# Optimization experiments

Hardware: AMD Instinct MI355X
Metric: run time of the kernel (lower is better)

The kernel has to match this reference:

```python
import jax, jax.numpy as jnp
import numpy as np

B, N, DIM, H = 8, 2048, 64, 8  # per-head dim == DIM (module convention: inner_dim = dim * n_heads)


def setup_inputs() -> dict:
    key = jax.random.key(0)
    k1, k2, k3 = jax.random.split(key, 3)
    x = jax.random.normal(k1, (B, N, DIM), dtype=jnp.float32)
    W_qkv = jax.random.normal(k2, (DIM, 3 * H * DIM), dtype=jnp.float32) * (DIM ** -0.5)
    W_out = jax.random.normal(k3, (H * DIM, DIM), dtype=jnp.float32) * ((H * DIM) ** -0.5)
    b_out = jnp.zeros((DIM,), dtype=jnp.float32)
    return {"x": x, "W_qkv": W_qkv, "W_out": W_out, "b_out": b_out}


def reference(x, W_qkv, W_out, b_out):
    b, n, d = x.shape
    h = W_qkv.shape[1] // (3 * d)
    qkv = x @ W_qkv                                   # [b, n, 3*h*d]
    q, k, v = jnp.split(qkv, 3, axis=-1)              # each [b, n, h*d]
    def to_heads(t):
        return t.reshape(b, n, h, d).transpose(0, 2, 1, 3)  # [b, h, n, d]
    q, k, v = map(to_heads, (q, k, v))
    scale = d ** -0.5
    dot = jnp.einsum('bhid,bhjd->bhij', q, k) * scale  # [b, h, n, n]
    A = jax.nn.softmax(dot, axis=-1)
    z = jnp.einsum('bhij,bhjd->bhid', A, v)            # [b, h, n, d]
    z = z.transpose(0, 2, 1, 3).reshape(b, n, h * d)   # [b, n, h*d]
    return z @ W_out + b_out                           # [b, n, d]
```

## Files before the change

### kernel.cpp

```cpp
#include <hip/hip_runtime.h>
#include <math.h>

#define BB 8
#define NN 2048
#define DD 64
#define HH 8
#define BH (BB*HH)
#define HD (HH*DD)
#define NROWS (BB*NN)
#define QKV_COLS (3*HD)

typedef __bf16 bf16_8 __attribute__((ext_vector_type(8)));
typedef __bf16 bf16_4 __attribute__((ext_vector_type(4)));
typedef float  f32_16 __attribute__((ext_vector_type(16)));
typedef float  f32_4  __attribute__((ext_vector_type(4)));
typedef int    i32_2  __attribute__((ext_vector_type(2)));

#define QSCALE 0.180336880111f

__device__ __forceinline__ unsigned pack_bf16(float a, float b) {
  union { __bf16 h[2]; unsigned u; } t;
  t.h[0] = (__bf16)a; t.h[1] = (__bf16)b;
  return t.u;
}

__device__ __forceinline__ float fast_exp2(float x) {
#if __has_builtin(__builtin_amdgcn_exp2f)
  return __builtin_amdgcn_exp2f(x);
#else
  return __expf(x * 0.69314718056f);
#endif
}

__device__ __forceinline__ bf16_8 half_swap(unsigned a0, unsigned a1,
                                            unsigned a2, unsigned a3,
                                            int lhi, int xl) {
  union { unsigned u[4]; bf16_8 v; } F;
#if __has_builtin(__builtin_amdgcn_permlane32_swap)
  i32_2 r02 = __builtin_amdgcn_permlane32_swap((int)a0, (int)a2, false, false);
  i32_2 r13 = __builtin_amdgcn_permlane32_swap((int)a1, (int)a3, false, false);
  F.u[0] = (unsigned)r02.x; F.u[2] = (unsigned)r02.y;
  F.u[1] = (unsigned)r13.x; F.u[3] = (unsigned)r13.y;
#else
  unsigned w0 = (unsigned)__shfl((int)a0, xl, 64);
  unsigned w1 = (unsigned)__shfl((int)a1, xl, 64);
  unsigned w2 = (unsigned)__shfl((int)a2, xl, 64);
  unsigned w3 = (unsigned)__shfl((int)a3, xl, 64);
  F.u[0] = lhi ? w2 : a0;
  F.u[1] = lhi ? w3 : a1;
  F.u[2] = lhi ? a2 : w0;
  F.u[3] = lhi ? a3 : w1;
#endif
  return F.v;
}

__global__ __launch_bounds__(256) void qkv_kernel(
    const float* __restrict__ x, const float* __restrict__ Wqkv,
    const float* __restrict__ Wout,
    __bf16* __restrict__ Q, __bf16* __restrict__ K, __bf16* __restrict__ Vt,
    __bf16* __restrict__ Wob) {
  __shared__ __bf16 T[4][64][34];

  if (blockIdx.y == (NROWS / 128)) {
    int id = blockIdx.x * 256 + threadIdx.x;
    for (int e = id; e < 512 * 64; e += 24 * 256) {
      int kf = e >> 6, col = e & 63;
      int s = kf >> 4, lh = (kf >> 3) & 1, j = kf & 7;
      int t = col >> 5, lc = col & 31;
      Wob[((size_t)((t * 32 + s) * 64 + lh * 32 + lc)) * 8 + j] = (__bf16)Wout[e];
    }
    return;
  }

  const int lane = threadIdx.x & 63;
  const int wave = threadIdx.x >> 6;
  const int l31  = lane & 31, lhi = lane >> 5;
  const int cg   = blockIdx.x;
  const int row0 = blockIdx.y * 128 + wave * 32;

  const float* xr = x + (size_t)(row0 + l31) * 64 + lhi * 8;
  bf16_8 af[4];
#pragma unroll
  for (int s = 0; s < 4; s++) {
    f32_4 a0 = *(const f32_4*)(xr + s * 16);
    f32_4 a1 = *(const f32_4*)(xr + s * 16 + 4);
#pragma unroll
    for (int j = 0; j < 4; j++) { af[s][j] = (__bf16)a0[j]; af[s][4 + j] = (__bf16)a1[j]; }
  }

  const int col0  = cg * 64;
  const int which = col0 >> 9;
  const float wscl = (which == 0) ? QSCALE : 1.0f;

  f32_16 C0, C1;
#pragma unroll
  for (int i = 0; i < 16; i++) { C0[i] = 0.f; C1[i] = 0.f; }

#pragma unroll
  for (int s = 0; s < 4; s++) {
    bf16_8 b0, b1;
#pragma unroll
    for (int j = 0; j < 8; j++) {
      int k = s * 16 + lhi * 8 + j;
      b0[j] = (__bf16)(Wqkv[(size_t)k * QKV_COLS + col0 + l31]      * wscl);
      b1[j] = (__bf16)(Wqkv[(size_t)k * QKV_COLS + col0 + 32 + l31] * wscl);
    }
    C0 = __builtin_amdgcn_mfma_f32_32x32x16_bf16(af[s], b0, C0, 0, 0, 0);
    C1 = __builtin_amdgcn_mfma_f32_32x32x16_bf16(af[s], b1, C1, 0, 0, 0);
  }

  const int h   = (col0 >> 6) & 7;
  const int b   = row0 >> 11;
  const int n0l = row0 & 2047;

  if (which < 2) {
    __bf16* dst = (which == 0) ? Q : K;
#pragma unroll
    for (int r = 0; r < 16; r++) {
      int nl = (r & 3) + 8 * (r >> 2) + 4 * lhi;
      size_t base = (((size_t)(b * HH + h) * NN) + n0l + nl) * DD;
      dst[base + l31]      = (__bf16)C0[r];
      dst[base + 32 + l31] = (__bf16)C1[r];
    }
  } else {
    __bf16 (*Tw)[34] = T[wave];
#pragma unroll
    for (int r = 0; r < 16; r++) {
      int nl = (r & 3) + 8 * (r >> 2) + 4 * lhi;
      Tw[l31][nl]      = (__bf16)C0[r];
      Tw[32 + l31][nl] = (__bf16)C1[r];
    }
    __bf16* dst = Vt + (((size_t)(b * HH + h) * DD) + lane) * NN + n0l;
#pragma unroll
    for (int j = 0; j < 4; j++) {
      *(bf16_8*)(dst + j * 8) = *(const bf16_8*)(&Tw[lane][j * 8]);
    }
  }
}

#define TILE_ELEMS (128 * 72 + 64 * 136)
__global__ __launch_bounds__(512) void attn_kernel(
    const __bf16* __restrict__ Q, const __bf16* __restrict__ K,
    const __bf16* __restrict__ Vt, __bf16* __restrict__ z) {
  __shared__ __bf16 SMEM[2][TILE_ELEMS];

  const int tid  = threadIdx.x;
  const int wave = tid >> 6;
  const int lane = tid & 63;
  const int l31  = lane & 31;
  const int lhi  = lane >> 5;
  const int xl   = lane ^ 32;
  const int bh   = blockIdx.x >> 2;
  const int q0   = (blockIdx.x & 3) * 512 + wave * 64;

  const __bf16* Qbase = Q + ((size_t)bh * NN + q0 + l31) * DD + lhi * 8;
  bf16_8 qfa[4], qfb[4];
#pragma unroll
  for (int s = 0; s < 4; s++) {
    qfa[s] = *(const bf16_8*)(Qbase + s * 16);
    qfb[s] = *(const bf16_8*)(Qbase + (size_t)32 * DD + s * 16);
  }

  f32_16 O0a, O1a, O0b, O1b;
#pragma unroll
  for (int i = 0; i < 16; i++) { O0a[i] = 0.f; O1a[i] = 0.f; O0b[i] = 0.f; O1b[i] = 0.f; }
  float lsa = 0.f, lsb = 0.f;

  const __bf16* Kb = K  + (size_t)bh * NN * DD;
  const __bf16* Vb = Vt + (size_t)bh * DD * NN;

  const int krow = tid >> 3, kcol = (tid & 7) * 8;
  const int vrow = tid >> 4, vcol = (tid & 15) * 8;
  const __bf16* kgl = Kb + (size_t)krow * 64 + kcol;
  const __bf16* vgl = Vb + (size_t)vrow * NN + vcol;
  const int koff0 = krow * 72 + kcol;
  const int voff0 = 128 * 72 + vrow * 136 + vcol;

  bf16_8 gk[2], gv[2];
#pragma unroll
  for (int i = 0; i < 2; i++) {
    gk[i] = *(const bf16_8*)(kgl + (size_t)i * 64 * 64);
    gv[i] = *(const bf16_8*)(vgl + (size_t)i * 32 * NN);
  }
  {
    __bf16* S = SMEM[0];
    *(bf16_8*)(S + koff0)            = gk[0];
    *(bf16_8*)(S + koff0 + 64 * 72)  = gk[1];
    *(bf16_8*)(S + voff0)            = gv[0];
    *(bf16_8*)(S + voff0 + 32 * 136) = gv[1];
  }
#pragma unroll
  for (int i = 0; i < 2; i++) {
    gk[i] = *(const bf16_8*)(kgl + (size_t)128 * 64 + (size_t)i * 64 * 64);
    gv[i] = *(const bf16_8*)(vgl + 128 + (size_t)i * 32 * NN);
  }
  __syncthreads();

  for (int it = 0; it < 16; it++) {
    __bf16* Ks = SMEM[it & 1];
    __bf16* Vs = SMEM[it & 1] + 128 * 72;

    if (it < 15) {
      __bf16* Sn = SMEM[(it + 1) & 1];
      *(bf16_8*)(Sn + koff0)            = gk[0];
      *(bf16_8*)(Sn + koff0 + 64 * 72)  = gk[1];
      *(bf16_8*)(Sn + voff0)            = gv[0];
      *(bf16_8*)(Sn + voff0 + 32 * 136) = gv[1];
      if (it < 14) {
        const size_t kadv = (size_t)(it + 2) * 128 * 64;
        const size_t vadv = (size_t)(it + 2) * 128;
#pragma unroll
        for (int i = 0; i < 2; i++) {
          gk[i] = *(const bf16_8*)(kgl + kadv + (size_t)i * 64 * 64);
          gv[i] = *(const bf16_8*)(vgl + vadv + (size_t)i * 32 * NN);
        }
      }
    }

#pragma unroll
    for (int hf = 0; hf < 2; hf++) {
      f32_16 S0a, S1a, S0b, S1b;
#pragma unroll
      for (int i = 0; i < 16; i++) { S0a[i] = 0.f; S1a[i] = 0.f; S0b[i] = 0.f; S1b[i] = 0.f; }
#pragma unroll
      for (int s = 0; s < 4; s++) {
        bf16_8 kb0 = *(const bf16_8*)(&Ks[(hf * 64 + l31) * 72 + s * 16 + lhi * 8]);
        bf16_8 kb1 = *(const bf16_8*)(&Ks[(hf * 64 + 32 + l31) * 72 + s * 16 + lhi * 8]);
        S0a = __builtin_amdgcn_mfma_f32_32x32x16_bf16(kb0, qfa[s], S0a, 0, 0, 0);
        S1a = __builtin_amdgcn_mfma_f32_32x32x16_bf16(kb1, qfa[s], S1a, 0, 0, 0);
        S0b = __builtin_amdgcn_mfma_f32_32x32x16_bf16(kb0, qfb[s], S0b, 0, 0, 0);
        S1b = __builtin_amdgcn_mfma_f32_32x32x16_bf16(kb1, qfb[s], S1b, 0, 0, 0);
      }

      unsigned pka[16], pkb[16];
#pragma unroll
      for (int t = 0; t < 8; t++) {
        float a0 = fast_exp2(S0a[2 * t]), a1 = fast_exp2(S0a[2 * t + 1]);
        float a2 = fast_exp2(S1a[2 * t]), a3 = fast_exp2(S1a[2 * t + 1]);
        lsa += (a0 + a1) + (a2 + a3);
        pka[t]     = pack_bf16(a0, a1);
        pka[8 + t] = pack_bf16(a2, a3);
        float b0 = fast_exp2(S0b[2 * t]), b1 = fast_exp2(S0b[2 * t + 1]);
        float b2 = fast_exp2(S1b[2 * t]), b3 = fast_exp2(S1b[2 * t + 1]);
        lsb += (b0 + b1) + (b2 + b3);
        pkb[t]     = pack_bf16(b0, b1);
        pkb[8 + t] = pack_bf16(b2, b3);
      }

#pragma unroll
      for (int g = 0; g < 4; g++) {
        const int base = (g >> 1) * 8 + (g & 1) * 4;
        bf16_8 va0 = *(const bf16_8*)(&Vs[l31 * 136 + hf * 64 + g * 16 + lhi * 8]);
        bf16_8 va1 = *(const bf16_8*)(&Vs[(32 + l31) * 136 + hf * 64 + g * 16 + lhi * 8]);
        bf16_8 Fa = half_swap(pka[base], pka[base + 1], pka[base + 2], pka[base + 3], lhi, xl);
        O0a = __builtin_amdgcn_mfma_f32_32x32x16_bf16(va0, Fa, O0a, 0, 0, 0);
        O1a = __builtin_amdgcn_mfma_f32_32x32x16_bf16(va1, Fa, O1a, 0, 0, 0);
        bf16_8 Fb = half_swap(pkb[base], pkb[base + 1], pkb[base + 2], pkb[base + 3], lhi, xl);
        O0b = __builtin_amdgcn_mfma_f32_32x32x16_bf16(va0, Fb, O0b, 0, 0, 0);
        O1b = __builtin_amdgcn_mfma_f32_32x32x16_bf16(va1, Fb, O1b, 0, 0, 0);
      }
    }
    __syncthreads();
  }

  lsa += __shfl_xor(lsa, 32, 64);
  lsb += __shfl_xor(lsb, 32, 64);
  const float inva = 1.f / lsa;
  const float invb = 1.f / lsb;

  const int b = bh >> 3, h = bh & 7;
  __bf16* ow = SMEM[0] + wave * (32 * 68);
  const int qr = lane >> 1, c0 = (lane & 1) * 32;
#pragma unroll
  for (int sub = 0; sub < 2; sub++) {
    const f32_16& P0 = sub ? O0b : O0a;
    const f32_16& P1 = sub ? O1b : O1a;
    const float inv = sub ? invb : inva;
#pragma unroll
    for (int g = 0; g < 4; g++) {
      bf16_4 p0, p1;
#pragma unroll
      for (int i = 0; i < 4; i++) {
        p0[i] = (__bf16)(P0[4 * g + i] * inv);
        p1[i] = (__bf16)(P1[4 * g + i] * inv);
      }
      const int d0 = 8 * g + 4 * lhi;
      *(bf16_4*)(ow + l31 * 68 + d0)      = p0;
      *(bf16_4*)(ow + l31 * 68 + 32 + d0) = p1;
    }
    __bf16* zp = z + ((size_t)b * NN + q0 + sub * 32 + qr) * HD + h * DD + c0;
#pragma unroll
    for (int j = 0; j < 4; j++) {
      *(bf16_8*)(zp + 8 * j) = *(const bf16_8*)(ow + qr * 68 + c0 + 8 * j);
    }
  }
}

__global__ __launch_bounds__(256) void out_proj_kernel(
    const __bf16* __restrict__ z, const __bf16* __restrict__ Wob,
    const float* __restrict__ bout, float* __restrict__ out) {
  __shared__ float red[3][64][33];
  const int tid  = threadIdx.x;
  const int wave = tid >> 6, lane = tid & 63;
  const int l31  = lane & 31, lhi = lane >> 5;
  const int row0 = blockIdx.x * 32;

  const __bf16* zr = z + (size_t)(row0 + l31) * HD + wave * 128 + lhi * 8;

  f32_16 C0, C1;
#pragma unroll
  for (int i = 0; i < 16; i++) { C0[i] = 0.f; C1[i] = 0.f; }

#pragma unroll
  for (int s = 0; s < 8; s++) {
    const int sa = wave * 8 + s;
    bf16_8 a  = *(const bf16_8*)(zr + s * 16);
    bf16_8 b0 = *(const bf16_8*)(Wob + ((size_t)((0 * 32 + sa) * 64 + lane)) * 8);
    bf16_8 b1 = *(const bf16_8*)(Wob + ((size_t)((1 * 32 + sa) * 64 + lane)) * 8);
    C0 = __builtin_amdgcn_mfma_f32_32x32x16_bf16(a, b0, C0, 0, 0, 0);
    C1 = __builtin_amdgcn_mfma_f32_32x32x16_bf16(a, b1, C1, 0, 0, 0);
  }

  if (wave) {
    float* rw = &red[wave - 1][lane][0];
#pragma unroll
    for (int r = 0; r < 16; r++) { rw[r] = C0[r]; rw[16 + r] = C1[r]; }
  }
  __syncthreads();
  if (wave == 0) {
    const float bi0 = bout[l31], bi1 = bout[32 + l31];
#pragma unroll
    for (int r = 0; r < 16; r++) {
      int n = row0 + (r & 3) + 8 * (r >> 2) + 4 * lhi;
      float v0 = C0[r] + red[0][lane][r]      + red[1][lane][r]      + red[2][lane][r];
      float v1 = C1[r] + red[0][lane][16 + r] + red[1][lane][16 + r] + red[2][lane][16 + r];
      out[(size_t)n * 64 + l31]      = v0 + bi0;
      out[(size_t)n * 64 + 32 + l31] = v1 + bi1;
    }
  }
}

extern "C" void kernel_launch(void* const* d_in, const int* in_sizes, int n_in,
                              void* d_out, int out_size, void* d_ws, size_t ws_size,
                              hipStream_t stream) {
  const float* x    = (const float*)d_in[0];
  const float* Wqkv = (const float*)d_in[1];
  const float* Wout = (const float*)d_in[2];
  const float* bout = (const float*)d_in[3];
  float* out = (float*)d_out;

  const size_t buf_elems = (size_t)BB * HH * NN * DD;
  __bf16* Qw  = (__bf16*)d_ws;
  __bf16* Kw  = Qw  + buf_elems;
  __bf16* Vtw = Kw  + buf_elems;
  __bf16* zw  = Vtw + buf_elems;
  __bf16* Wob = zw  + buf_elems;

  qkv_kernel<<<dim3(QKV_COLS / 64, NROWS / 128 + 1), 256, 0, stream>>>(
      x, Wqkv, Wout, Qw, Kw, Vtw, Wob);
  attn_kernel<<<BH * (NN / 512), 512, 0, stream>>>(Qw, Kw, Vtw, zw);
  out_proj_kernel<<<NROWS / 32, 256, 0, stream>>>(zw, Wob, bout, out);
}
```

Baseline: 180.0 us.

## Process keys in 32-wide groups to cut registers and allow two blocks per CU

The inner attention loop now handles 32 keys at a time instead of 64. This halves the live score accumulators and packed probability arrays, and the launch bounds now request two 512-thread blocks per CU to raise occupancy. The goal is to reduce register pressure so more waves can hide latency. In exchange, the code runs more loop iterations with shorter MFMA chains, and the register cap could cause spills.

Measured after the change: 168.8 us. 6.2% less time.

```diff
diff --git a/kernel.cpp b/kernel.cpp
--- a/kernel.cpp
+++ b/kernel.cpp
@@ -139,7 +139,7 @@
 }
 
 #define TILE_ELEMS (128 * 72 + 64 * 136)
-__global__ __launch_bounds__(512) void attn_kernel(
+__global__ __launch_bounds__(512, 2) void attn_kernel(
     const __bf16* __restrict__ Q, const __bf16* __restrict__ K,
     const __bf16* __restrict__ Vt, __bf16* __restrict__ z) {
   __shared__ __bf16 SMEM[2][TILE_ELEMS];
@@ -218,44 +218,39 @@
     }
 
 #pragma unroll
-    for (int hf = 0; hf < 2; hf++) {
-      f32_16 S0a, S1a, S0b, S1b;
-#pragma unroll
-      for (int i = 0; i < 16; i++) { S0a[i] = 0.f; S1a[i] = 0.f; S0b[i] = 0.f; S1b[i] = 0.f; }
+    for (int grp = 0; grp < 4; grp++) {
+      const int kb0 = grp * 32;
+
+      f32_16 Sa, Sb;
+#pragma unroll
+      for (int i = 0; i < 16; i++) { Sa[i] = 0.f; Sb[i] = 0.f; }
 #pragma unroll
       for (int s = 0; s < 4; s++) {
-        bf16_8 kb0 = *(const bf16_8*)(&Ks[(hf * 64 + l31) * 72 + s * 16 + lhi * 8]);
-        bf16_8 kb1 = *(const bf16_8*)(&Ks[(hf * 64 + 32 + l31) * 72 + s * 16 + lhi * 8]);
-        S0a = __builtin_amdgcn_mfma_f32_32x32x16_bf16(kb0, qfa[s], S0a, 0, 0, 0);
-        S1a = __builtin_amdgcn_mfma_f32_32x32x16_bf16(kb1, qfa[s], S1a, 0, 0, 0);
-        S0b = __builtin_amdgcn_mfma_f32_32x32x16_bf16(kb0, qfb[s], S0b, 0, 0, 0);
-        S1b = __builtin_amdgcn_mfma_f32_32x32x16_bf16(kb1, qfb[s], S1b, 0, 0, 0);
-      }
-
-      unsigned pka[16], pkb[16];
+        bf16_8 kb = *(const bf16_8*)(&Ks[(kb0 + l31) * 72 + s * 16 + lhi * 8]);
+        Sa = __builtin_amdgcn_mfma_f32_32x32x16_bf16(kb, qfa[s], Sa, 0, 0, 0);
+        Sb = __builtin_amdgcn_mfma_f32_32x32x16_bf16(kb, qfb[s], Sb, 0, 0, 0);
+      }
+
+      unsigned pka[8], pkb[8];
 #pragma unroll
       for (int t = 0; t < 8; t++) {
-        float a0 = fast_exp2(S0a[2 * t]), a1 = fast_exp2(S0a[2 * t + 1]);
-        float a2 = fast_exp2(S1a[2 * t]), a3 = fast_exp2(S1a[2 * t + 1]);
-        lsa += (a0 + a1) + (a2 + a3);
-        pka[t]     = pack_bf16(a0, a1);
-        pka[8 + t] = pack_bf16(a2, a3);
-        float b0 = fast_exp2(S0b[2 * t]), b1 = fast_exp2(S0b[2 * t + 1]);
-        float b2 = fast_exp2(S1b[2 * t]), b3 = fast_exp2(S1b[2 * t + 1]);
-        lsb += (b0 + b1) + (b2 + b3);
-        pkb[t]     = pack_bf16(b0, b1);
-        pkb[8 + t] = pack_bf16(b2, b3);
-      }
-
-#pragma unroll
-      for (int g = 0; g < 4; g++) {
-        const int base = (g >> 1) * 8 + (g & 1) * 4;
-        bf16_8 va0 = *(const bf16_8*)(&Vs[l31 * 136 + hf * 64 + g * 16 + lhi * 8]);
-        bf16_8 va1 = *(const bf16_8*)(&Vs[(32 + l31) * 136 + hf * 64 + g * 16 + lhi * 8]);
-        bf16_8 Fa = half_swap(pka[base], pka[base + 1], pka[base + 2], pka[base + 3], lhi, xl);
+        float a0 = fast_exp2(Sa[2 * t]), a1 = fast_exp2(Sa[2 * t + 1]);
+        lsa += a0 + a1;
+        pka[t] = pack_bf16(a0, a1);
+        float b0 = fast_exp2(Sb[2 * t]), b1 = fast_exp2(Sb[2 * t + 1]);
+        lsb += b0 + b1;
+        pkb[t] = pack_bf16(b0, b1);
+      }
+
+#pragma unroll
+      for (int g = 0; g < 2; g++) {
+        const int kc = kb0 + g * 16;
+        bf16_8 va0 = *(const bf16_8*)(&Vs[l31 * 136 + kc + lhi * 8]);
+        bf16_8 va1 = *(const bf16_8*)(&Vs[(32 + l31) * 136 + kc + lhi * 8]);
+        bf16_8 Fa = half_swap(pka[g * 4], pka[g * 4 + 1], pka[g * 4 + 2], pka[g * 4 + 3], lhi, xl);
         O0a = __builtin_amdgcn_mfma_f32_32x32x16_bf16(va0, Fa, O0a, 0, 0, 0);
         O1a = __builtin_amdgcn_mfma_f32_32x32x16_bf16(va1, Fa, O1a, 0, 0, 0);
-        bf16_8 Fb = half_swap(pkb[base], pkb[base + 1], pkb[base + 2], pkb[base + 3], lhi, xl);
+        bf16_8 Fb = half_swap(pkb[g * 4], pkb[g * 4 + 1], pkb[g * 4 + 2], pkb[g * 4 + 3], lhi, xl);
         O0b = __builtin_amdgcn_mfma_f32_32x32x16_bf16(va0, Fb, O0b, 0, 0, 0);
         O1b = __builtin_amdgcn_mfma_f32_32x32x16_bf16(va1, Fb, O1b, 0, 0, 0);
       }
```
